# Kernel tuning notes

Hardware: AMD Instinct MI355X
Metric: run time of the kernel (lower is better)

Reference implementation:

```python
import jax, jax.numpy as jnp
import numpy as np

DIM = 1024
HEADS = 16
HD = DIM // HEADS          # 64
HID = 4 * DIM              # 4096
TPF = 1374                 # tokens_per_frame
LR = 0.1
NS_ITERS = 5
TTT_STEPS = 2
B, S = 2, 4
SN = S * TPF               # 5496


def _newton_schulz(G, iters=NS_ITERS):
    """Muon Newton-Schulz orthogonalization (quintic iteration)."""
    a, b, c = 3.4445, -4.7750, 2.0315
    X = G / (jnp.linalg.norm(G) + 1e-7)
    transposed = G.shape[0] > G.shape[1]
    if transposed:
        X = X.T
    for _ in range(iters):
        A = X @ X.T                      # [m,m], m = min(rows, cols)
        X = a * X + (b * A + c * (A @ A)) @ X
    return X.T if transposed else X


def _muon_update(p, g):
    return p - LR * _newton_schulz(g)


def setup_inputs() -> dict:
    key = jax.random.key(0)
    ks = jax.random.split(key, 8)
    inp = {
        "x": jax.random.normal(ks[0], (B, SN, DIM), jnp.float32),
        "qkv_w": jax.random.normal(ks[1], (DIM, 3 * DIM), jnp.float32) * (DIM ** -0.5),
        "qkv_b": jnp.zeros((3 * DIM,), jnp.float32),
        "qn_scale": jnp.ones((HD,), jnp.float32),
        "qn_bias": jnp.zeros((HD,), jnp.float32),
        "kn_scale": jnp.ones((HD,), jnp.float32),
        "kn_bias": jnp.zeros((HD,), jnp.float32),
        # theta: lecun-normal scale (std = 1/sqrt(fan_in))
        "ttt_gate": jax.random.normal(ks[2], (DIM, HID), jnp.float32) * (DIM ** -0.5),
        "ttt_val": jax.random.normal(ks[3], (DIM, HID), jnp.float32) * (DIM ** -0.5),
        "ttt_proj": jax.random.normal(ks[4], (HID, DIM), jnp.float32) * (HID ** -0.5),
        "proj_w": jax.random.normal(ks[5], (DIM, DIM), jnp.float32) * (DIM ** -0.5),
        "proj_b": jnp.zeros((DIM,), jnp.float32),
    }
    return inp


def reference(x, qkv_w, qkv_b, qn_scale, qn_bias, kn_scale, kn_bias,
              ttt_gate, ttt_val, ttt_proj, proj_w, proj_b):
    Bx, SNx, _ = x.shape
    qkv = x @ qkv_w + qkv_b                       # [B, SN, 3*DIM]
    q, k, v = jnp.split(qkv, 3, axis=-1)
    q = q.reshape(Bx, SNx, HEADS, HD)
    k = k.reshape(Bx, SNx, HEADS, HD)
    # per-head L2 normalize then affine NormLayer (x*scale + bias)
    q = q / (jnp.linalg.norm(q, axis=-1, keepdims=True) + 1e-6) * qn_scale + qn_bias
    k = k / (jnp.linalg.norm(k, axis=-1, keepdims=True) + 1e-6) * kn_scale + kn_bias
    q_ttt = q.reshape(-1, DIM)                    # [B*SN, DIM]
    k_ttt = k.reshape(-1, DIM)
    # no short_conv param at init -> v_mixed is identity, so v_target == v
    v_ttt = v.reshape(-1, DIM)

    theta = {"gate": ttt_gate, "val": ttt_val, "proj": ttt_proj}

    def loss_fn(p):
        h = jax.nn.swish(k_ttt @ p["gate"]) * (k_ttt @ p["val"])   # [B*SN, HID]
        pred = h @ p["proj"]                                        # [B*SN, DIM]
        return jnp.mean((pred - v_ttt) ** 2)

    for _ in range(TTT_STEPS):
        grads = jax.grad(loss_fn)(theta)
        theta = {kk: _muon_update(theta[kk], grads[kk]) for kk in theta}

    h_q = jax.nn.swish(q_ttt @ theta["gate"]) * (q_ttt @ theta["val"])
    o = (h_q @ theta["proj"]) @ proj_w + proj_b
    return o.reshape(Bx, SNx, DIM)
```

## Files before the change

### kernel.cpp

```cpp
#include <hip/hip_runtime.h>
#include <stdint.h>

#define NTOK 10992
#define NTOKA 11264
#define FCHK 5632
#define PMi 4194304

typedef unsigned short u16;
typedef __attribute__((ext_vector_type(8))) __bf16 b8;
typedef __attribute__((ext_vector_type(4))) float f32x4;

__device__ __forceinline__ u16 f2b(float f) {
  union { float f; uint32_t u; } v; v.f = f;
  return (u16)((v.u + 0x7fffu + ((v.u >> 16) & 1u)) >> 16);
}
__device__ __forceinline__ float b2f(u16 b) {
  union { uint32_t u; float f; } v; v.u = ((uint32_t)b) << 16; return v.f;
}
__device__ __forceinline__ uint2 pk4(u16 a, u16 b, u16 c, u16 d) {
  uint2 r; r.x = (uint32_t)a | ((uint32_t)b << 16); r.y = (uint32_t)c | ((uint32_t)d << 16);
  return r;
}
__device__ __forceinline__ void gload16(const u16* g, u16* l) {
  __builtin_amdgcn_global_load_lds((const __attribute__((address_space(1))) void*)(const void*)g,
                                   (__attribute__((address_space(3))) void*)(void*)l, 16, 0, 0);
}

struct GA {
  const u16* A[3]; const u16* B[3];
  void* C[3]; u16* O1[3]; u16* OT[3];
  const void* E0[3]; const u16* E1[3];
  int lda[3], ldb[3];
  int M, N, K, ldc, ldo1, ldt, lde0, lde1;
  float p0, p1;
};

template <int EPI, int SPLIT>
__global__ __launch_bounds__(256, 2) void gemm_bt(GA g) {
  __shared__ u16 As[128 * 32];
  __shared__ u16 Bs[128 * 32];
  int bz = blockIdx.z, koff = 0, klen = g.K;
  if constexpr (SPLIT) { koff = (bz & 1) * (g.K >> 1); bz >>= 1; klen = g.K >> 1; }
  const u16* __restrict__ A = g.A[bz] + koff;
  const u16* __restrict__ B = g.B[bz] + koff;
  const int lda = g.lda[bz], ldb = g.ldb[bz];
  const int m0 = blockIdx.y * 128, n0 = blockIdx.x * 128;
  const int tid = threadIdx.x, w = tid >> 6, lane = tid & 63;
  const int wr = (w >> 1) * 64, wc = (w & 1) * 64;
  const int ln = lane & 15, lq = lane >> 4;

  f32x4 acc[4][4];
#pragma unroll
  for (int i = 0; i < 4; ++i)
#pragma unroll
    for (int j = 0; j < 4; ++j)
#pragma unroll
      for (int r = 0; r < 4; ++r) acc[i][j][r] = 0.f;

  const u16* Ag = A + (size_t)(m0 + 32 * w + (lane >> 2)) * lda + (lane & 3) * 8;
  const u16* Bg = B + (size_t)(n0 + 32 * w + (lane >> 2)) * ldb + (lane & 3) * 8;
  u16* AsW = &As[w * 1024];
  u16* BsW = &Bs[w * 1024];
  const int nkt = klen >> 5;

  for (int kt = 0; kt < nkt; ++kt) {
    __syncthreads();
    gload16(Ag, AsW);
    gload16(Ag + (size_t)16 * lda, AsW + 512);
    gload16(Bg, BsW);
    gload16(Bg + (size_t)16 * ldb, BsW + 512);
    Ag += 32; Bg += 32;
    __syncthreads();
    b8 af[4], bfr[4];
#pragma unroll
    for (int i = 0; i < 4; ++i) af[i] = *(const b8*)&As[(wr + i * 16 + ln) * 32 + lq * 8];
#pragma unroll
    for (int j = 0; j < 4; ++j) bfr[j] = *(const b8*)&Bs[(wc + j * 16 + ln) * 32 + lq * 8];
#pragma unroll
    for (int i = 0; i < 4; ++i)
#pragma unroll
      for (int j = 0; j < 4; ++j)
        acc[i][j] = __builtin_amdgcn_mfma_f32_16x16x32_bf16(af[i], bfr[j], acc[i][j], 0, 0, 0);
  }

  float* Cf = (float*)g.C[bz];
  u16* Cb = (u16*)g.C[bz];
  u16* O1 = g.O1[bz];
  u16* OT = g.OT[bz];
  const float* E0f = (const float*)g.E0[bz];
  const u16* E0b = (const u16*)g.E0[bz];
  const u16* E1b = g.E1[bz];

#pragma unroll
  for (int i = 0; i < 4; ++i) {
    const int mb = m0 + wr + i * 16 + lq * 4;
    if (mb >= g.M) continue;
#pragma unroll
    for (int j = 0; j < 4; ++j) {
      const int n = n0 + wc + j * 16 + ln;
      if (n >= g.N) continue;
      float vv[4];
#pragma unroll
      for (int r = 0; r < 4; ++r) vv[r] = acc[i][j][r];
      if constexpr (EPI == 0) {
#pragma unroll
        for (int r = 0; r < 4; ++r) Cb[(size_t)(mb + r) * g.ldc + n] = f2b(vv[r]);
      } else if constexpr (EPI == 1) {
        const float bias = E0f[n];
#pragma unroll
        for (int r = 0; r < 4; ++r) Cb[(size_t)(mb + r) * g.ldc + n] = f2b(vv[r] + bias);
      } else if constexpr (EPI == 5) {
        u16 cq[4], oq[4];
#pragma unroll
        for (int r = 0; r < 4; ++r) {
          const int m = mb + r;
          const float zg = b2f(E0b[(size_t)m * g.lde0 + n]);
          const float zv = b2f(E1b[(size_t)m * g.lde1 + n]);
          const float s = 1.f / (1.f + __expf(-zg));
          cq[r] = f2b(vv[r] * zv * s * (1.f + zg * (1.f - s)));
          oq[r] = f2b(vv[r] * zg * s);
        }
        *(uint2*)&Cb[(size_t)n * g.ldt + mb] = pk4(cq[0], cq[1], cq[2], cq[3]);
        *(uint2*)&O1[(size_t)n * g.ldt + mb] = pk4(oq[0], oq[1], oq[2], oq[3]);
      } else if constexpr (EPI == 8) {
#pragma unroll
        for (int r = 0; r < 4; ++r) atomicAdd(&Cf[(size_t)(mb + r) * g.ldc + n], vv[r]);
      } else if constexpr (EPI == 9) {
        u16 cq[4];
#pragma unroll
        for (int r = 0; r < 4; ++r) {
          const int m = mb + r;
          const u16 ub = f2b(g.p0 * b2f(E0b[(size_t)m * g.lde0 + n]) + vv[r]);
          Cb[(size_t)m * g.ldc + n] = ub;
          cq[r] = ub;
        }
        if (OT) *(uint2*)&OT[(size_t)n * g.ldt + mb] = pk4(cq[0], cq[1], cq[2], cq[3]);
      }
    }
  }
}

template <int EPI>
__global__ __launch_bounds__(256, 2) void gemm_gv(GA g) {
  __shared__ u16 As[128 * 32];
  __shared__ u16 Gs[128 * 32];
  __shared__ u16 Vs[128 * 32];
  const u16* __restrict__ A = g.A[0];
  const u16* __restrict__ G = g.B[0];
  const u16* __restrict__ V = g.B[1];
  const int lda = g.lda[0], ldb = g.ldb[0];
  const int m0 = blockIdx.y * 128, n0 = blockIdx.x * 128;
  const int tid = threadIdx.x, w = tid >> 6, lane = tid & 63;
  const int wr = (w >> 1) * 64, wc = (w & 1) * 64;
  const int ln = lane & 15, lq = lane >> 4;

  f32x4 ag[4][4], av[4][4];
#pragma unroll
  for (int i = 0; i < 4; ++i)
#pragma unroll
    for (int j = 0; j < 4; ++j)
#pragma unroll
      for (int r = 0; r < 4; ++r) { ag[i][j][r] = 0.f; av[i][j][r] = 0.f; }

  const u16* Agp = A + (size_t)(m0 + 32 * w + (lane >> 2)) * lda + (lane & 3) * 8;
  const u16* Ggp = G + (size_t)(n0 + 32 * w + (lane >> 2)) * ldb + (lane & 3) * 8;
  const u16* Vgp = V + (size_t)(n0 + 32 * w + (lane >> 2)) * ldb + (lane & 3) * 8;
  u16* AsW = &As[w * 1024];
  u16* GsW = &Gs[w * 1024];
  u16* VsW = &Vs[w * 1024];
  const int nkt = g.K >> 5;

  for (int kt = 0; kt < nkt; ++kt) {
    __syncthreads();
    gload16(Agp, AsW);
    gload16(Agp + (size_t)16 * lda, AsW + 512);
    gload16(Ggp, GsW);
    gload16(Ggp + (size_t)16 * ldb, GsW + 512);
    gload16(Vgp, VsW);
    gload16(Vgp + (size_t)16 * ldb, VsW + 512);
    Agp += 32; Ggp += 32; Vgp += 32;
    __syncthreads();
    b8 af[4], gf[4], vf[4];
#pragma unroll
    for (int i = 0; i < 4; ++i) af[i] = *(const b8*)&As[(wr + i * 16 + ln) * 32 + lq * 8];
#pragma unroll
    for (int j = 0; j < 4; ++j) gf[j] = *(const b8*)&Gs[(wc + j * 16 + ln) * 32 + lq * 8];
#pragma unroll
    for (int j = 0; j < 4; ++j) vf[j] = *(const b8*)&Vs[(wc + j * 16 + ln) * 32 + lq * 8];
#pragma unroll
    for (int i = 0; i < 4; ++i)
#pragma unroll
      for (int j = 0; j < 4; ++j) {
        ag[i][j] = __builtin_amdgcn_mfma_f32_16x16x32_bf16(af[i], gf[j], ag[i][j], 0, 0, 0);
        av[i][j] = __builtin_amdgcn_mfma_f32_16x16x32_bf16(af[i], vf[j], av[i][j], 0, 0, 0);
      }
  }

  u16* Zg = (u16*)g.C[0];
  u16* Zv = g.O1[0];
  u16* Hh = g.O1[1];
  u16* HT = g.OT[0];

#pragma unroll
  for (int i = 0; i < 4; ++i) {
    const int mb = m0 + wr + i * 16 + lq * 4;
    if (mb >= g.M) continue;
#pragma unroll
    for (int j = 0; j < 4; ++j) {
      const int n = n0 + wc + j * 16 + ln;
      if (n >= g.N) continue;
      u16 hq[4];
#pragma unroll
      for (int r = 0; r < 4; ++r) {
        const int m = mb + r;
        const float zg = ag[i][j][r];
        const float zv = av[i][j][r];
        const float s = 1.f / (1.f + __expf(-zg));
        const u16 hb = f2b(zg * s * zv);
        if constexpr (EPI == 0) {
          Zg[(size_t)m * g.ldc + n] = f2b(zg);
          Zv[(size_t)m * g.ldc + n] = f2b(zv);
          Hh[(size_t)m * g.ldc + n] = hb;
          hq[r] = hb;
        } else {
          Zg[(size_t)m * g.ldc + n] = hb;
        }
      }
      if constexpr (EPI == 0)
        *(uint2*)&HT[(size_t)n * g.ldt + mb] = pk4(hq[0], hq[1], hq[2], hq[3]);
    }
  }
}

__global__ __launch_bounds__(256, 2) void fused_gg(GA ggr, GA ggv, int ysplit) {
  __shared__ u16 As[128 * 32];
  __shared__ u16 Bs[128 * 32];
  __shared__ u16 Vs[128 * 32];
  const int tid = threadIdx.x, w = tid >> 6, lane = tid & 63;
  const int wr = (w >> 1) * 64, wc = (w & 1) * 64;
  const int ln = lane & 15, lq = lane >> 4;

  if ((int)blockIdx.y < ysplit) {
    const u16* __restrict__ A = ggv.A[0];
    const u16* __restrict__ G = ggv.B[0];
    const u16* __restrict__ V = ggv.B[1];
    const int lda = ggv.lda[0], ldb = ggv.ldb[0];
    const int m0 = blockIdx.y * 128, n0 = blockIdx.x * 128;
    f32x4 ag[4][4], av[4][4];
#pragma unroll
    for (int i = 0; i < 4; ++i)
#pragma unroll
      for (int j = 0; j < 4; ++j)
#pragma unroll
        for (int r = 0; r < 4; ++r) { ag[i][j][r] = 0.f; av[i][j][r] = 0.f; }
    const u16* Agp = A + (size_t)(m0 + 32 * w + (lane >> 2)) * lda + (lane & 3) * 8;
    const u16* Ggp = G + (size_t)(n0 + 32 * w + (lane >> 2)) * ldb + (lane & 3) * 8;
    const u16* Vgp = V + (size_t)(n0 + 32 * w + (lane >> 2)) * ldb + (lane & 3) * 8;
    u16* AsW = &As[w * 1024];
    u16* GsW = &Bs[w * 1024];
    u16* VsW = &Vs[w * 1024];
    const int nkt = ggv.K >> 5;
    for (int kt = 0; kt < nkt; ++kt) {
      __syncthreads();
      gload16(Agp, AsW);
      gload16(Agp + (size_t)16 * lda, AsW + 512);
      gload16(Ggp, GsW);
      gload16(Ggp + (size_t)16 * ldb, GsW + 512);
      gload16(Vgp, VsW);
      gload16(Vgp + (size_t)16 * ldb, VsW + 512);
      Agp += 32; Ggp += 32; Vgp += 32;
      __syncthreads();
      b8 af[4], gf[4], vf[4];
#pragma unroll
      for (int i = 0; i < 4; ++i) af[i] = *(const b8*)&As[(wr + i * 16 + ln) * 32 + lq * 8];
#pragma unroll
      for (int j = 0; j < 4; ++j) gf[j] = *(const b8*)&Bs[(wc + j * 16 + ln) * 32 + lq * 8];
#pragma unroll
      for (int j = 0; j < 4; ++j) vf[j] = *(const b8*)&Vs[(wc + j * 16 + ln) * 32 + lq * 8];
#pragma unroll
      for (int i = 0; i < 4; ++i)
#pragma unroll
        for (int j = 0; j < 4; ++j) {
          ag[i][j] = __builtin_amdgcn_mfma_f32_16x16x32_bf16(af[i], gf[j], ag[i][j], 0, 0, 0);
          av[i][j] = __builtin_amdgcn_mfma_f32_16x16x32_bf16(af[i], vf[j], av[i][j], 0, 0, 0);
        }
    }
    u16* Zg = (u16*)ggv.C[0];
    u16* Zv = ggv.O1[0];
    u16* Hh = ggv.O1[1];
    u16* HT = ggv.OT[0];
#pragma unroll
    for (int i = 0; i < 4; ++i) {
      const int mb = m0 + wr + i * 16 + lq * 4;
      if (mb >= ggv.M) continue;
#pragma unroll
      for (int j = 0; j < 4; ++j) {
        const int n = n0 + wc + j * 16 + ln;
        if (n >= ggv.N) continue;
        u16 hq[4];
#pragma unroll
        for (int r = 0; r < 4; ++r) {
          const int m = mb + r;
          const float zg = ag[i][j][r];
          const float zv = av[i][j][r];
          const float s = 1.f / (1.f + __expf(-zg));
          const u16 hb = f2b(zg * s * zv);
          Zg[(size_t)m * ggv.ldc + n] = f2b(zg);
          Zv[(size_t)m * ggv.ldc + n] = f2b(zv);
          Hh[(size_t)m * ggv.ldc + n] = hb;
          hq[r] = hb;
        }
        *(uint2*)&HT[(size_t)n * ggv.ldt + mb] = pk4(hq[0], hq[1], hq[2], hq[3]);
      }
    }
  } else {
    const int yy = (int)blockIdx.y - ysplit;
    int bz = yy >> 3;
    const int m0 = (yy & 7) * 128, n0 = blockIdx.x * 128;
    const int koff = (bz & 1) * (ggr.K >> 1); bz >>= 1;
    const int klen = ggr.K >> 1;
    const u16* __restrict__ A = ggr.A[bz] + koff;
    const u16* __restrict__ B = ggr.B[bz] + koff;
    const int lda = ggr.lda[bz], ldb = ggr.ldb[bz];
    f32x4 acc[4][4];
#pragma unroll
    for (int i = 0; i < 4; ++i)
#pragma unroll
      for (int j = 0; j < 4; ++j)
#pragma unroll
        for (int r = 0; r < 4; ++r) acc[i][j][r] = 0.f;
    const u16* Ag = A + (size_t)(m0 + 32 * w + (lane >> 2)) * lda + (lane & 3) * 8;
    const u16* Bg = B + (size_t)(n0 + 32 * w + (lane >> 2)) * ldb + (lane & 3) * 8;
    u16* AsW = &As[w * 1024];
    u16* BsW = &Bs[w * 1024];
    const int nkt = klen >> 5;
    for (int kt = 0; kt < nkt; ++kt) {
      __syncthreads();
      gload16(Ag, AsW);
      gload16(Ag + (size_t)16 * lda, AsW + 512);
      gload16(Bg, BsW);
      gload16(Bg + (size_t)16 * ldb, BsW + 512);
      Ag += 32; Bg += 32;
      __syncthreads();
      b8 af[4], bfr[4];
#pragma unroll
      for (int i = 0; i < 4; ++i) af[i] = *(const b8*)&As[(wr + i * 16 + ln) * 32 + lq * 8];
#pragma unroll
      for (int j = 0; j < 4; ++j) bfr[j] = *(const b8*)&Bs[(wc + j * 16 + ln) * 32 + lq * 8];
#pragma unroll
      for (int i = 0; i < 4; ++i)
#pragma unroll
        for (int j = 0; j < 4; ++j)
          acc[i][j] = __builtin_amdgcn_mfma_f32_16x16x32_bf16(af[i], bfr[j], acc[i][j], 0, 0, 0);
    }
    float* Cf = (float*)ggr.C[bz];
#pragma unroll
    for (int i = 0; i < 4; ++i) {
      const int mb = m0 + wr + i * 16 + lq * 4;
      if (mb >= ggr.M) continue;
#pragma unroll
      for (int j = 0; j < 4; ++j) {
        const int n = n0 + wc + j * 16 + ln;
        if (n >= ggr.N) continue;
#pragma unroll
        for (int r = 0; r < 4; ++r) atomicAdd(&Cf[(size_t)(mb + r) * ggr.ldc + n], acc[i][j][r]);
      }
    }
  }
}

template <int EPI>
__global__ __launch_bounds__(256, 2) void gemm64(GA g) {
  if constexpr (EPI == 10 || EPI == 11 || EPI == 12) {
    if (blockIdx.x > blockIdx.y) return;
  }
  __shared__ u16 As[64 * 32];
  __shared__ u16 Bs[64 * 32];
  const int bz = blockIdx.z;
  const u16* __restrict__ A = g.A[bz];
  const u16* __restrict__ B = g.B[bz];
  const int lda = g.lda[bz], ldb = g.ldb[bz];
  const int m0 = blockIdx.y * 64, n0 = blockIdx.x * 64;
  const int tid = threadIdx.x, w = tid >> 6, lane = tid & 63;
  const int wr = (w >> 1) * 32, wc = (w & 1) * 32;
  const int ln = lane & 15, lq = lane >> 4;

  f32x4 acc[2][2];
#pragma unroll
  for (int i = 0; i < 2; ++i)
#pragma unroll
    for (int j = 0; j < 2; ++j)
#pragma unroll
      for (int r = 0; r < 4; ++r) acc[i][j][r] = 0.f;

  const u16* Ag = A + (size_t)(m0 + 16 * w + (lane >> 2)) * lda + (lane & 3) * 8;
  const u16* Bg = B + (size_t)(n0 + 16 * w + (lane >> 2)) * ldb + (lane & 3) * 8;
  u16* AsW = &As[w * 512];
  u16* BsW = &Bs[w * 512];
  const int nkt = g.K >> 5;

  for (int kt = 0; kt < nkt; ++kt) {
    __syncthreads();
    gload16(Ag, AsW);
    gload16(Bg, BsW);
    Ag += 32; Bg += 32;
    __syncthreads();
    b8 af[2], bfr[2];
#pragma unroll
    for (int i = 0; i < 2; ++i) af[i] = *(const b8*)&As[(wr + i * 16 + ln) * 32 + lq * 8];
#pragma unroll
    for (int j = 0; j < 2; ++j) bfr[j] = *(const b8*)&Bs[(wc + j * 16 + ln) * 32 + lq * 8];
#pragma unroll
    for (int i = 0; i < 2; ++i)
#pragma unroll
      for (int j = 0; j < 2; ++j)
        acc[i][j] = __builtin_amdgcn_mfma_f32_16x16x32_bf16(af[i], bfr[j], acc[i][j], 0, 0, 0);
  }

  float* Cf = (float*)g.C[bz];
  u16* Cb = (u16*)g.C[bz];
  u16* OT = g.OT[bz];
  const float* E0f = (const float*)g.E0[bz];
  const u16* E0b = (const u16*)g.E0[bz];
  const u16* E1b = g.E1[bz];
  const bool offdiag = (blockIdx.x != blockIdx.y);

#pragma unroll
  for (int i = 0; i < 2; ++i) {
    const int mb = m0 + wr + i * 16 + lq * 4;
    if (mb >= g.M) continue;
#pragma unroll
    for (int j = 0; j < 2; ++j) {
      const int n = n0 + wc + j * 16 + ln;
      if (n >= g.N) continue;
      float vv[4];
#pragma unroll
      for (int r = 0; r < 4; ++r) vv[r] = acc[i][j][r];
      if constexpr (EPI == 0) {
#pragma unroll
        for (int r = 0; r < 4; ++r) Cb[(size_t)(mb + r) * g.ldc + n] = f2b(vv[r]);
      } else if constexpr (EPI == 2) {
        u16 cq[4];
#pragma unroll
        for (int r = 0; r < 4; ++r) {
          const int m = mb + r;
          const u16 ub = f2b((vv[r] - b2f(E0b[(size_t)m * g.lde0 + n])) * g.p0);
          Cb[(size_t)m * g.ldc + n] = ub;
          cq[r] = ub;
        }
        *(uint2*)&OT[(size_t)n * g.ldt + mb] = pk4(cq[0], cq[1], cq[2], cq[3]);
      } else if constexpr (EPI == 6) {
        const float bias = E0f[n];
#pragma unroll
        for (int r = 0; r < 4; ++r) Cf[(size_t)(mb + r) * g.ldc + n] = vv[r] + bias;
      } else if constexpr (EPI == 10) {
        u16 cq[4];
#pragma unroll
        for (int r = 0; r < 4; ++r) {
          cq[r] = f2b(vv[r]);
          Cb[(size_t)(mb + r) * g.ldc + n] = cq[r];
        }
        if (offdiag)
          *(uint2*)&Cb[(size_t)n * g.ldc + mb] = pk4(cq[0], cq[1], cq[2], cq[3]);
      } else if constexpr (EPI == 11) {
        u16 cq[4];
#pragma unroll
        for (int r = 0; r < 4; ++r) {
          cq[r] = f2b(g.p0 * b2f(E0b[(size_t)(mb + r) * g.lde0 + n]) + g.p1 * vv[r]);
          Cb[(size_t)(mb + r) * g.ldc + n] = cq[r];
        }
        if (offdiag)
          *(uint2*)&Cb[(size_t)n * g.ldc + mb] = pk4(cq[0], cq[1], cq[2], cq[3]);
      } else if constexpr (EPI == 12) {
        const uint2 t2u = *(const uint2*)&E1b[(size_t)n * g.lde1 + mb];
        const float t2v[4] = { b2f((u16)(t2u.x & 0xffff)), b2f((u16)(t2u.x >> 16)),
                               b2f((u16)(t2u.y & 0xffff)), b2f((u16)(t2u.y >> 16)) };
        u16 cq[4];
#pragma unroll
        for (int r = 0; r < 4; ++r) {
          const int m = mb + r;
          const float t1 = b2f(E1b[(size_t)m * g.lde1 + n]);
          const float a0 = b2f(E0b[(size_t)m * g.lde0 + n]);
          cq[r] = f2b(g.p0 * a0 + g.p1 * (t1 + t2v[r]) + vv[r]);
          Cb[(size_t)m * g.ldc + n] = cq[r];
        }
        if (offdiag)
          *(uint2*)&Cb[(size_t)n * g.ldc + mb] = pk4(cq[0], cq[1], cq[2], cq[3]);
      }
    }
  }
}

__global__ __launch_bounds__(256) void norm_qkv(const u16* __restrict__ qkvB,
    const float* __restrict__ qs, const float* __restrict__ qbi,
    const float* __restrict__ ks, const float* __restrict__ kbi,
    u16* __restrict__ qb, u16* __restrict__ kb, u16* __restrict__ vb) {
  const int tok = blockIdx.x;
  const int t = threadIdx.x;
  const int d = t * 4;
  const u16* row = qkvB + (size_t)tok * 3072;
  const uint2 qu = *(const uint2*)(row + d);
  const uint2 ku = *(const uint2*)(row + 1024 + d);
  *(uint2*)(vb + (size_t)tok * 1024 + d) = *(const uint2*)(row + 2048 + d);
  float q0 = b2f(qu.x & 0xffff), q1 = b2f(qu.x >> 16), q2 = b2f(qu.y & 0xffff), q3 = b2f(qu.y >> 16);
  float k0 = b2f(ku.x & 0xffff), k1 = b2f(ku.x >> 16), k2 = b2f(ku.y & 0xffff), k3 = b2f(ku.y >> 16);
  float sq = q0 * q0 + q1 * q1 + q2 * q2 + q3 * q3;
  float sk = k0 * k0 + k1 * k1 + k2 * k2 + k3 * k3;
  for (int off = 1; off < 16; off <<= 1) { sq += __shfl_xor(sq, off); sk += __shfl_xor(sk, off); }
  const float rq = 1.f / (sqrtf(sq) + 1e-6f);
  const float rk = 1.f / (sqrtf(sk) + 1e-6f);
  const int hd = d & 63;
  const float4 qsv = *(const float4*)(qs + hd);
  const float4 qbv = *(const float4*)(qbi + hd);
  const float4 ksv = *(const float4*)(ks + hd);
  const float4 kbv = *(const float4*)(kbi + hd);
  uint64_t pq = (uint64_t)f2b(q0 * rq * qsv.x + qbv.x)
              | ((uint64_t)f2b(q1 * rq * qsv.y + qbv.y) << 16)
              | ((uint64_t)f2b(q2 * rq * qsv.z + qbv.z) << 32)
              | ((uint64_t)f2b(q3 * rq * qsv.w + qbv.w) << 48);
  uint64_t pk = (uint64_t)f2b(k0 * rk * ksv.x + kbv.x)
              | ((uint64_t)f2b(k1 * rk * ksv.y + kbv.y) << 16)
              | ((uint64_t)f2b(k2 * rk * ksv.z + kbv.z) << 32)
              | ((uint64_t)f2b(k3 * rk * ksv.w + kbv.w) << 48);
  *(uint64_t*)(qb + (size_t)tok * 1024 + d) = pq;
  *(uint64_t*)(kb + (size_t)tok * 1024 + d) = pk;
}

__global__ __launch_bounds__(256) void tr_b16(const u16* __restrict__ in, u16* __restrict__ out,
                                              int Cin, int Rtot, int Rval,
                                              size_t inStr, size_t outStr) {
  const int b = blockIdx.z;
  in += (size_t)b * inStr; out += (size_t)b * outStr;
  __shared__ u16 t[32][33];
  const int c0 = blockIdx.x * 32, r0 = blockIdx.y * 32;
  const int tx = threadIdx.x, ty = threadIdx.y;
#pragma unroll
  for (int yy = 0; yy < 4; ++yy) {
    const int rr = ty * 4 + yy;
    const int r = r0 + rr;
    t[rr][tx] = (r < Rval) ? in[(size_t)r * Cin + c0 + tx] : (u16)0;
  }
  __syncthreads();
#pragma unroll
  for (int yy = 0; yy < 4; ++yy) {
    const int cc = ty * 4 + yy;
    out[(size_t)(c0 + cc) * Rtot + r0 + tx] = t[tx][cc];
  }
}

__global__ __launch_bounds__(256) void tr_f32b(const float* __restrict__ in, u16* __restrict__ out,
                                               int Cin, int Rtot) {
  __shared__ u16 t[32][33];
  const int c0 = blockIdx.x * 32, r0 = blockIdx.y * 32;
  const int tx = threadIdx.x, ty = threadIdx.y;
#pragma unroll
  for (int yy = 0; yy < 4; ++yy) {
    const int rr = ty * 4 + yy;
    t[rr][tx] = f2b(in[(size_t)(r0 + rr) * Cin + c0 + tx]);
  }
  __syncthreads();
#pragma unroll
  for (int yy = 0; yy < 4; ++yy) {
    const int cc = ty * 4 + yy;
    out[(size_t)(c0 + cc) * Rtot + r0 + tx] = t[tx][cc];
  }
}

__global__ void cvt_k(const float* __restrict__ in, u16* __restrict__ out, int n) {
  const int i = blockIdx.x * 256 + threadIdx.x;
  if (i < n) out[i] = f2b(in[i]);
}

__global__ void diag_k(float* __restrict__ out, int n, float val) {
  const int i = blockIdx.x * 256 + threadIdx.x;
  if (i < n) out[i] = val;
}

__global__ __launch_bounds__(256) void sumsq_k(const float* __restrict__ g, float* __restrict__ out) {
  const int b = blockIdx.y;
  const float* p = g + (size_t)b * PMi;
  float s = 0.f;
  for (int i = blockIdx.x * 256 + threadIdx.x; i < PMi; i += gridDim.x * 256) {
    float v = p[i]; s += v * v;
  }
  for (int off = 32; off > 0; off >>= 1) s += __shfl_xor(s, off);
  __shared__ float red[4];
  if ((threadIdx.x & 63) == 0) red[threadIdx.x >> 6] = s;
  __syncthreads();
  if (threadIdx.x == 0) atomicAdd(out + b, red[0] + red[1] + red[2] + red[3]);
}

__global__ __launch_bounds__(256) void scale_k(const float* __restrict__ g, const float* __restrict__ ss,
                                               u16* __restrict__ Xb) {
  const int b = blockIdx.y;
  const float r = 1.f / (sqrtf(ss[b]) + 1e-7f);
  const size_t o = (size_t)b * PMi;
  for (int i = blockIdx.x * 256 + threadIdx.x; i < PMi; i += gridDim.x * 256)
    Xb[o + i] = f2b(g[o + i] * r);
}

__global__ __launch_bounds__(256) void muon_apply(const u16* __restrict__ Xb_,
    u16* __restrict__ Gt, u16* __restrict__ Vt, u16* __restrict__ Pt, u16* __restrict__ Pb) {
  const int b = blockIdx.z;
  __shared__ float xs[32][33];
  __shared__ u16 ns[32][33];
  const int j0 = blockIdx.x * 32;
  const int i0 = blockIdx.y * 32;
  const u16* X = Xb_ + (size_t)b * PMi;
  const int tx = threadIdx.x, ty = threadIdx.y;
#pragma unroll
  for (int yy = 0; yy < 4; ++yy) {
    const int r = ty * 4 + yy;
    xs[r][tx] = b2f(X[(size_t)(i0 + r) * 4096 + j0 + tx]);
  }
  __syncthreads();
  if (b < 2) {
    u16* T = b ? Vt : Gt;
#pragma unroll
    for (int yy = 0; yy < 4; ++yy) {
      const int rr = ty * 4 + yy;
      const size_t idx = (size_t)(j0 + rr) * 1024 + i0 + tx;
      T[idx] = f2b(b2f(T[idx]) - 0.1f * xs[tx][rr]);
    }
  } else {
#pragma unroll
    for (int yy = 0; yy < 4; ++yy) {
      const int rr = ty * 4 + yy;
      const size_t idx = (size_t)(j0 + rr) * 1024 + i0 + tx;
      const float nv = b2f(Pb[idx]) - 0.1f * xs[tx][rr];
      const u16 nb = f2b(nv);
      Pb[idx] = nb;
      ns[rr][tx] = nb;
    }
    __syncthreads();
#pragma unroll
    for (int yy = 0; yy < 4; ++yy) {
      const int rr = ty * 4 + yy;
      Pt[(size_t)(i0 + rr) * 4096 + j0 + tx] = ns[tx][rr];
    }
  }
}

static GA mk(const u16* A, const u16* B, void* C, int M, int N, int K,
             int lda, int ldb, int ldc) {
  GA a{};
  a.A[0] = a.A[1] = a.A[2] = A;
  a.B[0] = a.B[1] = a.B[2] = B;
  a.C[0] = a.C[1] = a.C[2] = C;
  a.lda[0] = a.lda[1] = a.lda[2] = lda;
  a.ldb[0] = a.ldb[1] = a.ldb[2] = ldb;
  a.M = M; a.N = N; a.K = K; a.ldc = ldc;
  return a;
}

extern "C" void kernel_launch(void* const* d_in, const int* in_sizes, int n_in,
                              void* d_out, int out_size, void* d_ws, size_t ws_size,
                              hipStream_t stream) {
  (void)in_sizes; (void)n_in;
  const float* x      = (const float*)d_in[0];
  const float* qkv_w  = (const float*)d_in[1];
  const float* qkv_b  = (const float*)d_in[2];
  const float* qn_s   = (const float*)d_in[3];
  const float* qn_b   = (const float*)d_in[4];
  const float* kn_s   = (const float*)d_in[5];
  const float* kn_b   = (const float*)d_in[6];
  const float* g_gate = (const float*)d_in[7];
  const float* g_val  = (const float*)d_in[8];
  const float* g_proj = (const float*)d_in[9];
  const float* proj_w = (const float*)d_in[10];
  const float* proj_b = (const float*)d_in[11];
  float* out = (float*)d_out;

  const size_t PM = PMi;
  const size_t TD = (size_t)NTOKA * 1024;

  const size_t NEED1 = 253231360 + 4096;
  const size_t NEED2 = 127926528 + 177209344 + 4096;
  const size_t NEEDP = 351273216 + 8192;
  if (ws_size < NEED1) {
    diag_k<<<dim3((out_size + 255) / 256), dim3(256), 0, stream>>>(out, out_size,
                                                                   (float)(ws_size >> 20));
    return;
  }
  const int CHKr = (ws_size >= NEED2) ? 2816 : 1408;
  const int PAIRED = (ws_size >= NEEDP) ? 1 : 0;

  char* p = (char*)d_ws;
  auto carve = [&](size_t bytes) { char* r = p; p += (bytes + 255) & ~(size_t)255; return (void*)r; };
  auto cdiv = [](int a, int b) { return (a + b - 1) / b; };

  u16* Gt     = (u16*)carve(PM * 2);
  u16* Vt     = (u16*)carve(PM * 2);
  u16* Pt     = (u16*)carve(PM * 2);
  u16* Pb     = (u16*)carve(PM * 2);
  u16* projWt = (u16*)carve(1048576ull * 2);
  u16* qb     = (u16*)carve(TD * 2);
  u16* kb     = (u16*)carve(TD * 2);
  u16* vT     = (u16*)carve(TD * 2);
  u16* kT     = (u16*)carve(TD * 2);
  float* ssq  = (float*)carve(256);
  char* arena = p;

  u16* xb     = (u16*)arena;
  u16* qkvWt  = (u16*)(arena + 23068672);
  u16* qkvB   = (u16*)(arena + 29360128);
  u16* vb_tmp = (u16*)(arena + 96894976);
  const size_t CB = (size_t)CHKr * 4096 * 2;
  const size_t DP = (size_t)CHKr * 1024 * 2;
  u16* zg     = (u16*)arena;
  u16* zv     = (u16*)(arena + CB);
  u16* hh0    = (u16*)(arena + 2 * CB);
  u16* hT0    = (u16*)(arena + 3 * CB);
  u16* dzvT   = (u16*)(arena + 4 * CB);
  u16* dpredT = (u16*)(arena + 5 * CB);
  u16* dpredb = (u16*)(arena + 5 * CB + DP);
  float* gAll = (float*)(arena + 5 * CB + 2 * DP);
  u16* hh1    = PAIRED ? (u16*)(arena + 5 * CB + 2 * DP + 3 * PM * 4) : hh0;
  u16* hT1    = PAIRED ? (u16*)(arena + 6 * CB + 2 * DP + 3 * PM * 4) : hT0;
  u16* hhA[2] = {hh0, hh1};
  u16* hTA[2] = {hT0, hT1};
  u16* XAb  = (u16*)arena;
  u16* XAbT = (u16*)(arena + 25165824);
  u16* XBb  = (u16*)(arena + 50331648);
  u16* XBbT = (u16*)(arena + 75497472);
  u16* Ab   = (u16*)(arena + 100663296);
  u16* Wb   = (u16*)(arena + 106954752);
  u16* Tb   = (u16*)(arena + 113246208);
  const int FCN  = (CHKr >= 2816) ? 1 : 2;
  const int FBLK = (FCN == 1) ? NTOK : FCHK;
  u16* hbuf = (u16*)arena;
  u16* oc   = (u16*)(arena + ((FCN == 1) ? 92274688ull : 46137344ull));

  const dim3 blk(256), tb32(32, 8);
  const float inv2 = 2.0f / (10992.0f * 1024.0f);
  const float nsa = 3.4445f, nsb = -4.7750f, nsc = 2.0315f;

  cvt_k<<<dim3(43968), blk, 0, stream>>>(x, xb, NTOK * 1024);
  cvt_k<<<dim3(16384), blk, 0, stream>>>(g_proj, Pb, (int)PM);
  tr_f32b<<<dim3(96, 32), tb32, 0, stream>>>(qkv_w, qkvWt, 3072, 1024);
  tr_f32b<<<dim3(32, 32), tb32, 0, stream>>>(proj_w, projWt, 1024, 1024);
  tr_f32b<<<dim3(128, 32), tb32, 0, stream>>>(g_gate, Gt, 4096, 1024);
  tr_f32b<<<dim3(128, 32), tb32, 0, stream>>>(g_val, Vt, 4096, 1024);
  tr_f32b<<<dim3(32, 128), tb32, 0, stream>>>(g_proj, Pt, 1024, 4096);

  {
    GA a = mk(xb, qkvWt, qkvB, NTOK, 3072, 1024, 1024, 1024, 3072);
    a.E0[0] = a.E0[1] = a.E0[2] = qkv_b;
    gemm_bt<1, 0><<<dim3(24, 86, 1), blk, 0, stream>>>(a);
  }
  norm_qkv<<<dim3(NTOK), blk, 0, stream>>>(qkvB, qn_s, qn_b, kn_s, kn_b, qb, kb, vb_tmp);
  tr_b16<<<dim3(32, 352, 1), tb32, 0, stream>>>(kb, kT, 1024, NTOKA, NTOK, 0, 0);
  tr_b16<<<dim3(32, 352, 1), tb32, 0, stream>>>(vb_tmp, vT, 1024, NTOKA, NTOK, 0, 0);

  for (int step = 0; step < 2; ++step) {
    hipMemsetAsync(gAll, 0, 3 * PM * 4, stream);
    int havePend = 0;
    GA pendGA{};
    for (int ci = 0, c0 = 0; c0 < NTOK; ++ci, c0 += CHKr) {
      const int vc = (NTOK - c0 < CHKr) ? (NTOK - c0) : CHKr;
      const int mt = cdiv(vc, 128);
      const u16* kc = kb + (size_t)c0 * 1024;
      u16* hhp = hhA[ci & 1];
      u16* hTp = hTA[ci & 1];
      if (vc < CHKr)
        hipMemsetAsync(hTp, 0, CB, stream);
      {
        GA agv{};
        agv.A[0] = kc; agv.lda[0] = 1024;
        agv.B[0] = Gt; agv.B[1] = Vt; agv.ldb[0] = 1024;
        agv.C[0] = zg; agv.O1[0] = zv; agv.O1[1] = hhp; agv.OT[0] = hTp;
        agv.M = vc; agv.N = 4096; agv.K = 1024; agv.ldc = 4096; agv.ldt = CHKr;
        if (PAIRED && havePend) {
          fused_gg<<<dim3(32, mt + 48, 1), blk, 0, stream>>>(pendGA, agv, mt);
          havePend = 0;
        } else {
          gemm_gv<0><<<dim3(32, mt, 1), blk, 0, stream>>>(agv);
        }
      }
      if (vc < CHKr) {
        hipMemsetAsync(dzvT, 0, CB, stream);
        hipMemsetAsync(dpredT, 0, DP, stream);
      }
      {
        GA a = mk(Pt, hhp, dpredT, 1024, vc, 4096, 4096, 4096, CHKr);
        a.OT[0] = dpredb; a.ldt = 1024;
        a.E0[0] = vT + c0; a.lde0 = NTOKA; a.p0 = inv2;
        gemm64<2><<<dim3(cdiv(vc, 64), 16, 1), blk, 0, stream>>>(a);
      }
      if (vc < CHKr)
        hipMemsetAsync(hhp, 0, CB, stream);
      {
        GA a = mk(dpredb, Pb, hhp, vc, 4096, 1024, 1024, 1024, 0);
        a.O1[0] = dzvT; a.ldt = CHKr;
        a.E0[0] = zg; a.lde0 = 4096; a.E1[0] = zv; a.lde1 = 4096;
        gemm_bt<5, 0><<<dim3(32, mt, 1), blk, 0, stream>>>(a);
      }
      {
        GA a{};
        a.A[0] = kT + c0; a.A[1] = kT + c0; a.A[2] = dpredT;
        a.lda[0] = NTOKA; a.lda[1] = NTOKA; a.lda[2] = CHKr;
        a.B[0] = hhp; a.B[1] = dzvT; a.B[2] = hTp;
        a.ldb[0] = a.ldb[1] = a.ldb[2] = CHKr;
        a.C[0] = gAll; a.C[1] = gAll + PM; a.C[2] = gAll + 2 * PM;
        a.M = 1024; a.N = 4096; a.K = CHKr; a.ldc = 4096;
        const int last = (c0 + CHKr >= NTOK);
        if (PAIRED && !last) { pendGA = a; havePend = 1; }
        else gemm_bt<8, 1><<<dim3(32, 8, 6), blk, 0, stream>>>(a);
      }
    }
    hipMemsetAsync(ssq, 0, 16, stream);
    sumsq_k<<<dim3(512, 3), blk, 0, stream>>>(gAll, ssq);
    scale_k<<<dim3(2048, 3), blk, 0, stream>>>(gAll, ssq, XAb);
    tr_b16<<<dim3(128, 32, 3), tb32, 0, stream>>>(XAb, XAbT, 4096, 1024, 1024, PM, PM);

    u16* Xi_b = XAb; u16* Xi_bT = XAbT;
    u16* Xo_b = XBb; u16* Xo_bT = XBbT;
    {
      GA a{};
      for (int b = 0; b < 3; ++b) {
        a.A[b] = Xi_b + (size_t)b * PM; a.B[b] = Xi_b + (size_t)b * PM;
        a.C[b] = Ab + (size_t)b * 1048576;
        a.lda[b] = 4096; a.ldb[b] = 4096;
      }
      a.M = 1024; a.N = 1024; a.K = 4096; a.ldc = 1024;
      gemm64<10><<<dim3(16, 16, 3), blk, 0, stream>>>(a);
    }
    for (int it = 0; it < 5; ++it) {
      {
        GA a{};
        for (int b = 0; b < 3; ++b) {
          a.A[b] = Ab + (size_t)b * 1048576; a.B[b] = Ab + (size_t)b * 1048576;
          a.C[b] = Wb + (size_t)b * 1048576; a.E0[b] = Ab + (size_t)b * 1048576;
          a.lda[b] = 1024; a.ldb[b] = 1024;
        }
        a.M = 1024; a.N = 1024; a.K = 1024; a.ldc = 1024; a.lde0 = 1024;
        a.p0 = nsb; a.p1 = nsc;
        gemm64<11><<<dim3(16, 16, 3), blk, 0, stream>>>(a);
      }
      {
        GA a{};
        for (int b = 0; b < 3; ++b) {
          a.A[b] = Wb + (size_t)b * 1048576; a.B[b] = Xi_bT + (size_t)b * PM;
          a.C[b] = Xo_b + (size_t)b * PM;
          a.OT[b] = (it == 4) ? nullptr : (Xo_bT + (size_t)b * PM);
          a.E0[b] = Xi_b + (size_t)b * PM;
          a.lda[b] = 1024; a.ldb[b] = 1024;
        }
        a.M = 1024; a.N = 4096; a.K = 1024; a.ldc = 4096; a.ldt = 1024;
        a.lde0 = 4096; a.p0 = nsa;
        gemm_bt<9, 0><<<dim3(32, 8, 3), blk, 0, stream>>>(a);
      }
      if (it < 4) {
        {
          GA a{};
          for (int b = 0; b < 3; ++b) {
            a.A[b] = Wb + (size_t)b * 1048576; a.B[b] = Ab + (size_t)b * 1048576;
            a.C[b] = Tb + (size_t)b * 1048576;
            a.lda[b] = 1024; a.ldb[b] = 1024;
          }
          a.M = 1024; a.N = 1024; a.K = 1024; a.ldc = 1024;
          gemm64<0><<<dim3(16, 16, 3), blk, 0, stream>>>(a);
        }
        {
          GA a{};
          for (int b = 0; b < 3; ++b) {
            a.A[b] = Tb + (size_t)b * 1048576; a.B[b] = Wb + (size_t)b * 1048576;
            a.C[b] = Ab + (size_t)b * 1048576;
            a.E0[b] = Ab + (size_t)b * 1048576; a.E1[b] = Tb + (size_t)b * 1048576;
            a.lda[b] = 1024; a.ldb[b] = 1024;
          }
          a.M = 1024; a.N = 1024; a.K = 1024; a.ldc = 1024;
          a.lde0 = 1024; a.lde1 = 1024;
          a.p0 = nsa * nsa; a.p1 = nsa;
          gemm64<12><<<dim3(16, 16, 3), blk, 0, stream>>>(a);
        }
      }
      u16* tb = Xi_b; Xi_b = Xo_b; Xo_b = tb;
      u16* tt = Xi_bT; Xi_bT = Xo_bT; Xo_bT = tt;
    }
    muon_apply<<<dim3(128, 32, 3), tb32, 0, stream>>>(Xi_b, Gt, Vt, Pt, Pb);
  }

  for (int fc = 0; fc < FCN; ++fc) {
    const int c0 = fc * FBLK;
    const int vc = (NTOK - c0 < FBLK) ? (NTOK - c0) : FBLK;
    const int mt = cdiv(vc, 128), mt64 = cdiv(vc, 64);
    const u16* qc = qb + (size_t)c0 * 1024;
    {
      GA a{};
      a.A[0] = qc; a.lda[0] = 1024;
      a.B[0] = Gt; a.B[1] = Vt; a.ldb[0] = 1024;
      a.C[0] = hbuf;
      a.M = vc; a.N = 4096; a.K = 1024; a.ldc = 4096;
      gemm_gv<1><<<dim3(32, mt, 1), blk, 0, stream>>>(a);
    }
    gemm64<0><<<dim3(16, mt64, 1), blk, 0, stream>>>(
        mk(hbuf, Pt, oc, vc, 1024, 4096, 4096, 4096, 1024));
    {
      GA a = mk(oc, projWt, out + (size_t)c0 * 1024, vc, 1024, 1024, 1024, 1024, 1024);
      a.E0[0] = proj_b;
      gemm64<6><<<dim3(16, mt64, 1), blk, 0, stream>>>(a);
    }
  }
}
```

Before: 6.079 ms.

## Fold proj_w into TTT proj, fuse NS gemms, fuse scale+transpose

Precomputes the product of the updated TTT projection and proj_w once (4096x1024). The final per-token path then becomes a single K=4096 GEMM instead of two chained GEMMs with an intermediate buffer. Inside the Newton-Schulz loop, the X-update GEMM and the W*A GEMM now run in one launch split across the grid, and the normalisation scale is fused with the transpose. The workspace sizing logic is reworked so paired mode can run with smaller chunk sizes. Extra bf16 rounding of the folded weight may shift numerics slightly.

```diff
diff --git a/kernel.cpp b/kernel.cpp
--- a/kernel.cpp
+++ b/kernel.cpp
@@ -369,6 +369,121 @@
   }
 }
 
+__global__ __launch_bounds__(256, 2) void fused_xt(GA gx, GA gt) {
+  __shared__ u16 As[128 * 32];
+  __shared__ u16 Bs[128 * 32];
+  const int tid = threadIdx.x, w = tid >> 6, lane = tid & 63;
+  const int ln = lane & 15, lq = lane >> 4;
+  const int bz = blockIdx.z;
+
+  if ((int)blockIdx.y < 8) {
+    const int wr = (w >> 1) * 64, wc = (w & 1) * 64;
+    const u16* __restrict__ A = gx.A[bz];
+    const u16* __restrict__ B = gx.B[bz];
+    const int lda = gx.lda[bz], ldb = gx.ldb[bz];
+    const int m0 = blockIdx.y * 128, n0 = blockIdx.x * 128;
+    f32x4 acc[4][4];
+#pragma unroll
+    for (int i = 0; i < 4; ++i)
+#pragma unroll
+      for (int j = 0; j < 4; ++j)
+#pragma unroll
+        for (int r = 0; r < 4; ++r) acc[i][j][r] = 0.f;
+    const u16* Ag = A + (size_t)(m0 + 32 * w + (lane >> 2)) * lda + (lane & 3) * 8;
+    const u16* Bg = B + (size_t)(n0 + 32 * w + (lane >> 2)) * ldb + (lane & 3) * 8;
+    u16* AsW = &As[w * 1024];
+    u16* BsW = &Bs[w * 1024];
+    const int nkt = gx.K >> 5;
+    for (int kt = 0; kt < nkt; ++kt) {
+      __syncthreads();
+      gload16(Ag, AsW);
+      gload16(Ag + (size_t)16 * lda, AsW + 512);
+      gload16(Bg, BsW);
+      gload16(Bg + (size_t)16 * ldb, BsW + 512);
+      Ag += 32; Bg += 32;
+      __syncthreads();
+      b8 af[4], bfr[4];
+#pragma unroll
+      for (int i = 0; i < 4; ++i) af[i] = *(const b8*)&As[(wr + i * 16 + ln) * 32 + lq * 8];
+#pragma unroll
+      for (int j = 0; j < 4; ++j) bfr[j] = *(const b8*)&Bs[(wc + j * 16 + ln) * 32 + lq * 8];
+#pragma unroll
+      for (int i = 0; i < 4; ++i)
+#pragma unroll
+        for (int j = 0; j < 4; ++j)
+          acc[i][j] = __builtin_amdgcn_mfma_f32_16x16x32_bf16(af[i], bfr[j], acc[i][j], 0, 0, 0);
+    }
+    u16* Cb = (u16*)gx.C[bz];
+    u16* OT = gx.OT[bz];
+    const u16* E0b = (const u16*)gx.E0[bz];
+#pragma unroll
+    for (int i = 0; i < 4; ++i) {
+      const int mb = m0 + wr + i * 16 + lq * 4;
+#pragma unroll
+      for (int j = 0; j < 4; ++j) {
+        const int n = n0 + wc + j * 16 + ln;
+        u16 cq[4];
+#pragma unroll
+        for (int r = 0; r < 4; ++r) {
+          const int m = mb + r;
+          const u16 ub = f2b(gx.p0 * b2f(E0b[(size_t)m * gx.lde0 + n]) + acc[i][j][r]);
+          Cb[(size_t)m * gx.ldc + n] = ub;
+          cq[r] = ub;
+        }
+        if (OT) *(uint2*)&OT[(size_t)n * gx.ldt + mb] = pk4(cq[0], cq[1], cq[2], cq[3]);
+      }
+    }
+  } else {
+    const int wr = (w >> 1) * 32, wc = (w & 1) * 32;
+    const int tx16 = blockIdx.x >> 1;
+    const int ty16 = ((blockIdx.y - 8) << 1) | (blockIdx.x & 1);
+    const int m0 = ty16 * 64, n0 = tx16 * 64;
+    const u16* __restrict__ A = gt.A[bz];
+    const u16* __restrict__ B = gt.B[bz];
+    const int lda = gt.lda[bz], ldb = gt.ldb[bz];
+    f32x4 acc[2][2];
+#pragma unroll
+    for (int i = 0; i < 2; ++i)
+#pragma unroll
+      for (int j = 0; j < 2; ++j)
+#pragma unroll
+        for (int r = 0; r < 4; ++r) acc[i][j][r] = 0.f;
+    const u16* Ag = A + (size_t)(m0 + 16 * w + (lane >> 2)) * lda + (lane & 3) * 8;
+    const u16* Bg = B + (size_t)(n0 + 16 * w + (lane >> 2)) * ldb + (lane & 3) * 8;
+    u16* AsW = &As[w * 512];
+    u16* BsW = &Bs[w * 512];
+    const int nkt = gt.K >> 5;
+    for (int kt = 0; kt < nkt; ++kt) {
+      __syncthreads();
+      gload16(Ag, AsW);
+      gload16(Bg, BsW);
+      Ag += 32; Bg += 32;
+      __syncthreads();
+      b8 af[2], bfr[2];
+#pragma unroll
+      for (int i = 0; i < 2; ++i) af[i] = *(const b8*)&As[(wr + i * 16 + ln) * 32 + lq * 8];
+#pragma unroll
+      for (int j = 0; j < 2; ++j) bfr[j] = *(const b8*)&Bs[(wc + j * 16 + ln) * 32 + lq * 8];
+#pragma unroll
+      for (int i = 0; i < 2; ++i)
+#pragma unroll
+        for (int j = 0; j < 2; ++j)
+          acc[i][j] = __builtin_amdgcn_mfma_f32_16x16x32_bf16(af[i], bfr[j], acc[i][j], 0, 0, 0);
+    }
+    u16* Cb = (u16*)gt.C[bz];
+#pragma unroll
+    for (int i = 0; i < 2; ++i) {
+      const int mb = m0 + wr + i * 16 + lq * 4;
+#pragma unroll
+      for (int j = 0; j < 2; ++j) {
+        const int n = n0 + wc + j * 16 + ln;
+#pragma unroll
+        for (int r = 0; r < 4; ++r) Cb[(size_t)(mb + r) * gt.ldc + n] = f2b(acc[i][j][r]);
+      }
+    }
+  }
+}
+
 template <int EPI>
 __global__ __launch_bounds__(256, 2) void gemm64(GA g) {
   if constexpr (EPI == 10 || EPI == 11 || EPI == 12) {
@@ -436,10 +551,7 @@
       float vv[4];
 #pragma unroll
       for (int r = 0; r < 4; ++r) vv[r] = acc[i][j][r];
-      if constexpr (EPI == 0) {
-#pragma unroll
-        for (int r = 0; r < 4; ++r) Cb[(size_t)(mb + r) * g.ldc + n] = f2b(vv[r]);
-      } else if constexpr (EPI == 2) {
+      if constexpr (EPI == 2) {
         u16 cq[4];
 #pragma unroll
         for (int r = 0; r < 4; ++r) {
@@ -590,13 +702,29 @@
   if (threadIdx.x == 0) atomicAdd(out + b, red[0] + red[1] + red[2] + red[3]);
 }
 
-__global__ __launch_bounds__(256) void scale_k(const float* __restrict__ g, const float* __restrict__ ss,
-                                               u16* __restrict__ Xb) {
-  const int b = blockIdx.y;
+__global__ __launch_bounds__(256) void scale_tr(const float* __restrict__ g, const float* __restrict__ ss,
+                                                u16* __restrict__ Xb, u16* __restrict__ XbT) {
+  const int b = blockIdx.z;
+  __shared__ u16 t[32][33];
   const float r = 1.f / (sqrtf(ss[b]) + 1e-7f);
-  const size_t o = (size_t)b * PMi;
-  for (int i = blockIdx.x * 256 + threadIdx.x; i < PMi; i += gridDim.x * 256)
-    Xb[o + i] = f2b(g[o + i] * r);
+  const float* G = g + (size_t)b * PMi;
+  u16* X = Xb + (size_t)b * PMi;
+  u16* XT = XbT + (size_t)b * PMi;
+  const int j0 = blockIdx.x * 32, i0 = blockIdx.y * 32;
+  const int tx = threadIdx.x, ty = threadIdx.y;
+#pragma unroll
+  for (int yy = 0; yy < 4; ++yy) {
+    const int rr = ty * 4 + yy;
+    const u16 v = f2b(G[(size_t)(i0 + rr) * 4096 + j0 + tx] * r);
+    X[(size_t)(i0 + rr) * 4096 + j0 + tx] = v;
+    t[rr][tx] = v;
+  }
+  __syncthreads();
+#pragma unroll
+  for (int yy = 0; yy < 4; ++yy) {
+    const int cc = ty * 4 + yy;
+    XT[(size_t)(j0 + cc) * 1024 + i0 + tx] = t[tx][cc];
+  }
 }
 
 __global__ __launch_bounds__(256) void muon_apply(const u16* __restrict__ Xb_,
@@ -673,17 +801,23 @@
 
   const size_t PM = PMi;
   const size_t TD = (size_t)NTOKA * 1024;
-
+  const size_t PERS = 127926528ull;
+
+  auto needP = [&](int chk) {
+    return PERS + 7ull * (size_t)chk * 8192 + 2ull * (size_t)chk * 2048 + 50331648ull + 8192;
+  };
   const size_t NEED1 = 253231360 + 4096;
-  const size_t NEED2 = 127926528 + 177209344 + 4096;
-  const size_t NEEDP = 351273216 + 8192;
-  if (ws_size < NEED1) {
+  int CHKr, PAIRED;
+  if      (ws_size >= needP(2816)) { CHKr = 2816; PAIRED = 1; }
+  else if (ws_size >= needP(2560)) { CHKr = 2560; PAIRED = 1; }
+  else if (ws_size >= needP(2304)) { CHKr = 2304; PAIRED = 1; }
+  else if (ws_size >= needP(2048)) { CHKr = 2048; PAIRED = 1; }
+  else if (ws_size >= NEED1)       { CHKr = 1408; PAIRED = 0; }
+  else {
     diag_k<<<dim3((out_size + 255) / 256), dim3(256), 0, stream>>>(out, out_size,
                                                                    (float)(ws_size >> 20));
     return;
   }
-  const int CHKr = (ws_size >= NEED2) ? 2816 : 1408;
-  const int PAIRED = (ws_size >= NEEDP) ? 1 : 0;
 
   char* p = (char*)d_ws;
   auto carve = [&](size_t bytes) { char* r = p; p += (bytes + 255) & ~(size_t)255; return (void*)r; };
@@ -726,10 +860,10 @@
   u16* Ab   = (u16*)(arena + 100663296);
   u16* Wb   = (u16*)(arena + 106954752);
   u16* Tb   = (u16*)(arena + 113246208);
-  const int FCN  = (CHKr >= 2816) ? 1 : 2;
+  const int FCN  = PAIRED ? 1 : 2;
   const int FBLK = (FCN == 1) ? NTOK : FCHK;
   u16* hbuf = (u16*)arena;
-  u16* oc   = (u16*)(arena + ((FCN == 1) ? 92274688ull : 46137344ull));
+  u16* PWt  = (u16*)(arena + ((FCN == 1) ? 92274688ull : 46137344ull));
 
   const dim3 blk(256), tb32(32, 8);
   const float inv2 = 2.0f / (10992.0f * 1024.0f);
@@ -810,8 +944,7 @@
     }
     hipMemsetAsync(ssq, 0, 16, stream);
     sumsq_k<<<dim3(512, 3), blk, 0, stream>>>(gAll, ssq);
-    scale_k<<<dim3(2048, 3), blk, 0, stream>>>(gAll, ssq, XAb);
-    tr_b16<<<dim3(128, 32, 3), tb32, 0, stream>>>(XAb, XAbT, 4096, 1024, 1024, PM, PM);
+    scale_tr<<<dim3(128, 32, 3), tb32, 0, stream>>>(gAll, ssq, XAb, XAbT);
 
     u16* Xi_b = XAb; u16* Xi_bT = XAbT;
     u16* Xo_b = XBb; u16* Xo_bT = XBbT;
@@ -837,30 +970,25 @@
         a.p0 = nsb; a.p1 = nsc;
         gemm64<11><<<dim3(16, 16, 3), blk, 0, stream>>>(a);
       }
-      {
-        GA a{};
+      GA ax{};
+      for (int b = 0; b < 3; ++b) {
+        ax.A[b] = Wb + (size_t)b * 1048576; ax.B[b] = Xi_bT + (size_t)b * PM;
+        ax.C[b] = Xo_b + (size_t)b * PM;
+        ax.OT[b] = (it == 4) ? nullptr : (Xo_bT + (size_t)b * PM);
+        ax.E0[b] = Xi_b + (size_t)b * PM;
+        ax.lda[b] = 1024; ax.ldb[b] = 1024;
+      }
+      ax.M = 1024; ax.N = 4096; ax.K = 1024; ax.ldc = 4096; ax.ldt = 1024;
+      ax.lde0 = 4096; ax.p0 = nsa;
+      if (it < 4) {
+        GA at{};
         for (int b = 0; b < 3; ++b) {
-          a.A[b] = Wb + (size_t)b * 1048576; a.B[b] = Xi_bT + (size_t)b * PM;
-          a.C[b] = Xo_b + (size_t)b * PM;
-          a.OT[b] = (it == 4) ? nullptr : (Xo_bT + (size_t)b * PM);
-          a.E0[b] = Xi_b + (size_t)b * PM;
-          a.lda[b] = 1024; a.ldb[b] = 1024;
-        }
-        a.M = 1024; a.N = 4096; a.K = 1024; a.ldc = 4096; a.ldt = 1024;
-        a.lde0 = 4096; a.p0 = nsa;
-        gemm_bt<9, 0><<<dim3(32, 8, 3), blk, 0, stream>>>(a);
-      }
-      if (it < 4) {
-        {
-          GA a{};
-          for (int b = 0; b < 3; ++b) {
-            a.A[b] = Wb + (size_t)b * 1048576; a.B[b] = Ab + (size_t)b * 1048576;
-            a.C[b] = Tb + (size_t)b * 1048576;
-            a.lda[b] = 1024; a.ldb[b] = 1024;
-          }
-          a.M = 1024; a.N = 1024; a.K = 1024; a.ldc = 1024;
-          gemm64<0><<<dim3(16, 16, 3), blk, 0, stream>>>(a);
-        }
+          at.A[b] = Wb + (size_t)b * 1048576; at.B[b] = Ab + (size_t)b * 1048576;
+          at.C[b] = Tb + (size_t)b * 1048576;
+          at.lda[b] = 1024; at.ldb[b] = 1024;
+        }
+        at.M = 1024; at.N = 1024; at.K = 1024; at.ldc = 1024;
+        fused_xt<<<dim3(32, 16, 3), blk, 0, stream>>>(ax, at);
         {
           GA a{};
           for (int b = 0; b < 3; ++b) {
@@ -874,6 +1002,8 @@
           a.p0 = nsa * nsa; a.p1 = nsa;
           gemm64<12><<<dim3(16, 16, 3), blk, 0, stream>>>(a);
         }
+      } else {
+        gemm_bt<9, 0><<<dim3(32, 8, 3), blk, 0, stream>>>(ax);
       }
       u16* tb = Xi_b; Xi_b = Xo_b; Xo_b = tb;
       u16* tt = Xi_bT; Xi_bT = Xo_bT; Xo_bT = tt;
@@ -881,6 +1011,8 @@
     muon_apply<<<dim3(128, 32, 3), tb32, 0, stream>>>(Xi_b, Gt, Vt, Pt, Pb);
   }
 
+  gemm_bt<0, 0><<<dim3(32, 8, 1), blk, 0, stream>>>(
+      mk(projWt, Pb, PWt, 1024, 4096, 1024, 1024, 1024, 4096));
   for (int fc = 0; fc < FCN; ++fc) {
     const int c0 = fc * FBLK;
     const int vc = (NTOK - c0 < FBLK) ? (NTOK - c0) : FBLK;
@@ -894,10 +1026,8 @@
       a.M = vc; a.N = 4096; a.K = 1024; a.ldc = 4096;
       gemm_gv<1><<<dim3(32, mt, 1), blk, 0, stream>>>(a);
     }
-    gemm64<0><<<dim3(16, mt64, 1), blk, 0, stream>>>(
-        mk(hbuf, Pt, oc, vc, 1024, 4096, 4096, 4096, 1024));
     {
-      GA a = mk(oc, projWt, out + (size_t)c0 * 1024, vc, 1024, 1024, 1024, 1024, 1024);
+      GA a = mk(hbuf, PWt, out + (size_t)c0 * 1024, vc, 1024, 4096, 4096, 4096, 1024);
       a.E0[0] = proj_b;
       gemm64<6><<<dim3(16, mt64, 1), blk, 0, stream>>>(a);
     }
```

Result: no change. 5.982 ms (-1.6%).
